# Kernel tuning notes

Hardware: AMD Instinct MI355X
Metric: run time of the kernel (lower is better)

Reference implementation:

```python
import jax, jax.numpy as jnp
import numpy as np

N = 100000
E = 3200000
IN_F = 256
OUT_F = 64
ALPHA = 0.2  # LeakyReLU negative slope


def setup_inputs() -> dict:
    key = jax.random.key(0)
    k1, k2, k3, k4 = jax.random.split(key, 4)
    adj = jax.random.randint(k1, (2, E), 0, N, dtype=jnp.int64)
    x = jax.random.normal(k2, (N, IN_F), dtype=jnp.float32)
    # xavier-normal-ish scales
    W_fc = jax.random.normal(k3, (OUT_F, IN_F), dtype=jnp.float32) * (1.414 * np.sqrt(2.0 / (IN_F + OUT_F)))
    b_fc = jnp.zeros((OUT_F,), dtype=jnp.float32)
    a = jax.random.normal(k4, (1, 2 * OUT_F), dtype=jnp.float32) * (1.414 * np.sqrt(2.0 / (1 + 2 * OUT_F)))
    return {"adj": adj, "x": x, "W_fc": W_fc, "b_fc": b_fc, "a": a}


def reference(adj, x, W_fc, b_fc, a):
    src = adj[0]  # [E]
    dst = adj[1]  # [E]
    h = x @ W_fc.T + b_fc                       # [N, OUT_F]
    a1, a2 = a[0, :OUT_F], a[0, OUT_F:]         # split of attention vector
    # e = leakyrelu(a . [h_src || h_dst]) computed without materializing concat
    s1 = h @ a1                                  # [N]
    s2 = h @ a2                                  # [N]
    e = s1[src] + s2[dst]                        # [E]
    e = jnp.where(e > 0, e, ALPHA * e)           # LeakyReLU
    # dgl edge_softmax: softmax over edges grouped by destination node
    m = jax.ops.segment_max(e, dst, num_segments=N)     # [N]
    ex = jnp.exp(e - m[dst])                             # [E]
    denom = jax.ops.segment_sum(ex, dst, num_segments=N) # [N]
    att = ex / denom[dst]                                # [E]
    # SparseTensor(row=src, col=dst, value=att) @ h -> out[src] += att * h[dst]
    h_prime = jax.ops.segment_sum(att[:, None] * h[dst], src, num_segments=N)  # [N, OUT_F]
    return jax.nn.elu(h_prime)  # concat=True branch
```

## Files before the change

kernel.cpp:

```cpp
#include <hip/hip_runtime.h>
#include <math.h>

#define N_NODES 100000
#define N_EDGES 3200000
#define IN_F 256
#define OUT_F 64
#define LRELU_ALPHA 0.2f
#define NBKT 782
#define CAP 4480

typedef unsigned short u16;
typedef __attribute__((ext_vector_type(8))) short short8;
typedef __attribute__((ext_vector_type(4))) float floatx4;

__device__ inline u16 f2bf(float f) {
  unsigned u = __float_as_uint(f);
  u += 0x7FFFu + ((u >> 16) & 1u);
  return (u16)(u >> 16);
}
__device__ inline float bf2f(u16 h) {
  return __uint_as_float(((unsigned)h) << 16);
}

__global__ __launch_bounds__(256) void k_prep(const float* __restrict__ W,
                                              u16* __restrict__ Wbf,
                                              int* __restrict__ sfill,
                                              int* __restrict__ dfill) {
  if (blockIdx.x < 64) {
    int i = blockIdx.x * 256 + threadIdx.x;
    Wbf[i] = f2bf(W[i]);
  } else {
    for (int i = threadIdx.x; i < NBKT; i += 256) {
      sfill[i] = 0;
      dfill[i] = 0;
    }
  }
}

__global__ __launch_bounds__(256) void k_linear(
    const float* __restrict__ x, const u16* __restrict__ Wbf,
    const float* __restrict__ b, const float* __restrict__ a,
    u16* __restrict__ hbf, float* __restrict__ s1, float* __restrict__ s2) {
  __shared__ u16 Wlds[64 * 264];

  const int t = threadIdx.x;
#pragma unroll
  for (int p = 0; p < 8; p++) {
    int c = p * 256 + t;
    int row = c >> 5;
    int kc = (c & 31) * 8;
    *(short8*)&Wlds[row * 264 + kc] = *(const short8*)&Wbf[row * 256 + kc];
  }
  __syncthreads();

  const int w = t >> 6;
  const int lane = t & 63;
  const int col = lane & 15;
  const int q = lane >> 4;
  const int m0 = blockIdx.x * 64 + w * 16;

  floatx4 acc[4];
#pragma unroll
  for (int nt = 0; nt < 4; nt++) acc[nt] = (floatx4){0.f, 0.f, 0.f, 0.f};

  int mrow = m0 + col;
  if (mrow > N_NODES - 1) mrow = N_NODES - 1;
  const float* xrow = x + (size_t)mrow * IN_F + q * 8;

#pragma unroll
  for (int kk = 0; kk < 8; kk++) {
    float4 f0 = *(const float4*)(xrow + kk * 32);
    float4 f1 = *(const float4*)(xrow + kk * 32 + 4);
    short8 af;
    af[0] = (short)f2bf(f0.x);
    af[1] = (short)f2bf(f0.y);
    af[2] = (short)f2bf(f0.z);
    af[3] = (short)f2bf(f0.w);
    af[4] = (short)f2bf(f1.x);
    af[5] = (short)f2bf(f1.y);
    af[6] = (short)f2bf(f1.z);
    af[7] = (short)f2bf(f1.w);
#pragma unroll
    for (int nt = 0; nt < 4; nt++) {
      short8 bfr = *(const short8*)&Wlds[(nt * 16 + col) * 264 + kk * 32 + q * 8];
      acc[nt] = __builtin_amdgcn_mfma_f32_16x16x32_bf16(af, bfr, acc[nt], 0, 0, 0);
    }
  }

  float bv[4], a1v[4], a2v[4];
#pragma unroll
  for (int nt = 0; nt < 4; nt++) {
    bv[nt] = b[nt * 16 + col];
    a1v[nt] = a[nt * 16 + col];
    a2v[nt] = a[OUT_F + nt * 16 + col];
  }
#pragma unroll
  for (int r = 0; r < 4; r++) {
    int node = m0 + q * 4 + r;
    float p1 = 0.f, p2 = 0.f;
#pragma unroll
    for (int nt = 0; nt < 4; nt++) {
      float hv = acc[nt][r] + bv[nt];
      if (node < N_NODES) hbf[(size_t)node * OUT_F + nt * 16 + col] = f2bf(hv);
      p1 = fmaf(hv, a1v[nt], p1);
      p2 = fmaf(hv, a2v[nt], p2);
    }
#pragma unroll
    for (int s = 1; s < 16; s <<= 1) {
      p1 += __shfl_xor(p1, s, 16);
      p2 += __shfl_xor(p2, s, 16);
    }
    if (col == 0 && node < N_NODES) {
      s1[node] = p1;
      s2[node] = p2;
    }
  }
}

#define PBT 512
#define EPT_P 8
#define PEB (PBT * EPT_P)
__global__ __launch_bounds__(PBT) void k_place(
    const int* __restrict__ src, const int* __restrict__ dst,
    const float* __restrict__ s1, const float* __restrict__ s2,
    int* __restrict__ sfill, int* __restrict__ dfill,
    float2* __restrict__ pairS, float2* __restrict__ pairD) {
  __shared__ int lc[NBKT];
  __shared__ int ofs[NBKT];
  __shared__ int gbase[NBKT];
  __shared__ int tot;
  __shared__ float2 stage[PEB];
  __shared__ u16 stageB[PEB];

  const int t = threadIdx.x;
  const int base = blockIdx.x * PEB + t;

  float ex[EPT_P];
  int pk[EPT_P];
  int bs[EPT_P];

  for (int i = t; i < NBKT; i += PBT) lc[i] = 0;
  if (t == 0) tot = 0;
  __syncthreads();

#pragma unroll
  for (int j = 0; j < EPT_P; j++) {
    int e = base + j * PBT;
    if (e < N_EDGES) {
      int s = src[e];
      int d = dst[e];
      float v = s1[s] + s2[d];
      v = v > 0.f ? v : LRELU_ALPHA * v;
      ex[j] = __expf(v);
      pk[j] = d | ((s & 127) << 17);
      bs[j] = s >> 7;
      atomicAdd(&lc[bs[j]], 1);
    } else {
      bs[j] = -1;
    }
  }
  __syncthreads();

  for (int i = t; i < NBKT; i += PBT) {
    int c = lc[i];
    if (c) {
      gbase[i] = i * CAP + atomicAdd(&sfill[i], c);
      ofs[i] = atomicAdd(&tot, c);
    }
  }
  __syncthreads();
  const int nval = tot;
  for (int i = t; i < NBKT; i += PBT) lc[i] = 0;
  __syncthreads();

#pragma unroll
  for (int j = 0; j < EPT_P; j++) {
    if (bs[j] >= 0) {
      int r = atomicAdd(&lc[bs[j]], 1);
      int idx = ofs[bs[j]] + r;
      stage[idx] = make_float2(ex[j], __int_as_float(pk[j]));
      stageB[idx] = (u16)bs[j];
    }
  }
  __syncthreads();

  for (int i = t; i < nval; i += PBT) {
    int bkt = stageB[i];
    pairS[gbase[bkt] + (i - ofs[bkt])] = stage[i];
  }
  __syncthreads();

  for (int i = t; i < NBKT; i += PBT) lc[i] = 0;
  if (t == 0) tot = 0;
  __syncthreads();
#pragma unroll
  for (int j = 0; j < EPT_P; j++) {
    if (bs[j] >= 0) {
      int bd = (pk[j] & 0x1FFFF) >> 7;
      atomicAdd(&lc[bd], 1);
    }
  }
  __syncthreads();

  for (int i = t; i < NBKT; i += PBT) {
    int c = lc[i];
    if (c) {
      gbase[i] = i * CAP + atomicAdd(&dfill[i], c);
      ofs[i] = atomicAdd(&tot, c);
    }
  }
  __syncthreads();
  for (int i = t; i < NBKT; i += PBT) lc[i] = 0;
  __syncthreads();

#pragma unroll
  for (int j = 0; j < EPT_P; j++) {
    if (bs[j] >= 0) {
      int d = pk[j] & 0x1FFFF;
      int bd = d >> 7;
      int r = atomicAdd(&lc[bd], 1);
      int idx = ofs[bd] + r;
      stage[idx] = make_float2(ex[j], __int_as_float(d & 127));
      stageB[idx] = (u16)bd;
    }
  }
  __syncthreads();

  for (int i = t; i < nval; i += PBT) {
    int bkt = stageB[i];
    pairD[gbase[bkt] + (i - ofs[bkt])] = stage[i];
  }
}

__global__ __launch_bounds__(256) void k_denom(const int* __restrict__ dfill,
                                               const float2* __restrict__ pairD,
                                               float* __restrict__ denom_r) {
  __shared__ float lacc[128];
  const int t = threadIdx.x;
  const int bkt = blockIdx.x;
  if (t < 128) lacc[t] = 0.f;
  __syncthreads();
  int beg = bkt * CAP;
  int end = beg + dfill[bkt];
  for (int i = beg + t; i < end; i += 256) {
    float2 p = pairD[i];
    atomicAdd(&lacc[__float_as_int(p.y)], p.x);
  }
  __syncthreads();
  if (t < 128) {
    int node = bkt * 128 + t;
    if (node < N_NODES) denom_r[node] = 1.0f / lacc[t];
  }
}

#define SAT 512
__global__ __launch_bounds__(SAT) void k_sortagg(
    const int* __restrict__ sfill, const float2* __restrict__ pairS,
    const float* __restrict__ denom_r, const u16* __restrict__ hbf,
    float* __restrict__ out) {
  __shared__ float2 stg[CAP];
  __shared__ int lcnt[128];
  __shared__ int cur[128];
  __shared__ int nbeg[128];
  __shared__ int nend[128];
  __shared__ int w0tot;
  const int t = threadIdx.x;
  const int bkt = blockIdx.x;

  if (t < 128) lcnt[t] = 0;
  __syncthreads();

  const int gbeg = bkt * CAP;
  const int ne = sfill[bkt];

  for (int i = t; i < ne; i += SAT) {
    int pkv = __float_as_int(pairS[gbeg + i].y);
    atomicAdd(&lcnt[(pkv >> 17) & 127], 1);
  }
  __syncthreads();

  const int lane = t & 63;
  int v = (t < 128) ? lcnt[t] : 0;
  int val = v;
#pragma unroll
  for (int o = 1; o < 64; o <<= 1) {
    int u = __shfl_up(val, o, 64);
    if (lane >= o) val += u;
  }
  if (t == 63) w0tot = val;
  __syncthreads();
  if (t < 128) {
    int excl = val - v + ((t >= 64) ? w0tot : 0);
    cur[t] = excl;
    nbeg[t] = excl;
    nend[t] = excl + v;
  }
  __syncthreads();

  for (int i = t; i < ne; i += SAT) {
    float2 p = pairS[gbeg + i];
    int pkv = __float_as_int(p.y);
    int sl = (pkv >> 17) & 127;
    int d = pkv & 0x1FFFF;
    float att = p.x * denom_r[d];
    int pos = atomicAdd(&cur[sl], 1);
    stg[pos] = make_float2(att, __int_as_float(d));
  }
  __syncthreads();

  const int G = t >> 4;
  const int sl = t & 15;
  for (int nl = G; nl < 128; nl += 32) {
    int node = bkt * 128 + nl;
    int i = nbeg[nl];
    const int e0 = nend[nl];
    float4 acc = make_float4(0.f, 0.f, 0.f, 0.f);
    for (; i + 1 < e0; i += 2) {
      float2 p0 = stg[i];
      float2 p1 = stg[i + 1];
      int d0 = __float_as_int(p0.y);
      int d1 = __float_as_int(p1.y);
      ushort4 q0 = *(const ushort4*)&hbf[(size_t)d0 * OUT_F + sl * 4];
      ushort4 q1 = *(const ushort4*)&hbf[(size_t)d1 * OUT_F + sl * 4];
      acc.x = fmaf(p0.x, bf2f(q0.x), acc.x);
      acc.y = fmaf(p0.x, bf2f(q0.y), acc.y);
      acc.z = fmaf(p0.x, bf2f(q0.z), acc.z);
      acc.w = fmaf(p0.x, bf2f(q0.w), acc.w);
      acc.x = fmaf(p1.x, bf2f(q1.x), acc.x);
      acc.y = fmaf(p1.x, bf2f(q1.y), acc.y);
      acc.z = fmaf(p1.x, bf2f(q1.z), acc.z);
      acc.w = fmaf(p1.x, bf2f(q1.w), acc.w);
    }
    if (i < e0) {
      float2 p = stg[i];
      int d = __float_as_int(p.y);
      ushort4 q = *(const ushort4*)&hbf[(size_t)d * OUT_F + sl * 4];
      acc.x = fmaf(p.x, bf2f(q.x), acc.x);
      acc.y = fmaf(p.x, bf2f(q.y), acc.y);
      acc.z = fmaf(p.x, bf2f(q.z), acc.z);
      acc.w = fmaf(p.x, bf2f(q.w), acc.w);
    }
    if (node < N_NODES) {
      float4 o;
      o.x = acc.x > 0.f ? acc.x : expm1f(acc.x);
      o.y = acc.y > 0.f ? acc.y : expm1f(acc.y);
      o.z = acc.z > 0.f ? acc.z : expm1f(acc.z);
      o.w = acc.w > 0.f ? acc.w : expm1f(acc.w);
      *(float4*)(out + (size_t)node * OUT_F + sl * 4) = o;
    }
  }
}

extern "C" void kernel_launch(void* const* d_in, const int* in_sizes, int n_in,
                              void* d_out, int out_size, void* d_ws,
                              size_t ws_size, hipStream_t stream) {
  const int* adj = (const int*)d_in[0];
  const float* x = (const float*)d_in[1];
  const float* W = (const float*)d_in[2];
  const float* b = (const float*)d_in[3];
  const float* a = (const float*)d_in[4];
  float* out = (float*)d_out;

  float* ws = (float*)d_ws;
  float* s1v = ws;
  float* s2v = ws + 100000;
  float* denom_r = ws + 200000;
  int* sfill = (int*)(ws + 300000);
  int* dfill = (int*)(ws + 300800);
  float2* pairS = (float2*)(ws + 301600);
  float2* pairD = (float2*)(ws + 7308320);
  u16* hbf = (u16*)(ws + 14315040);
  u16* Wbf = (u16*)(ws + 17515040);

  const int* src = adj;
  const int* dst = adj + N_EDGES;

  k_prep<<<65, 256, 0, stream>>>(W, Wbf, sfill, dfill);
  k_linear<<<(N_NODES + 63) / 64, 256, 0, stream>>>(x, Wbf, b, a, hbf, s1v, s2v);
  k_place<<<(N_EDGES + PEB - 1) / PEB, PBT, 0, stream>>>(
      src, dst, s1v, s2v, sfill, dfill, pairS, pairD);
  k_denom<<<NBKT, 256, 0, stream>>>(dfill, pairD, denom_r);
  k_sortagg<<<NBKT, SAT, 0, stream>>>(sfill, pairS, denom_r, hbf, out);
}
```

Measured before the change: 369.9 us.

## Split edge placement into two grid halves and pack dst-side pairs into 32 bits

The placement kernel now runs on a 2-D grid: one half of the blocks buckets edges by source, the other by destination, instead of each block doing both passes in sequence. This doubles block-level parallelism and drops the second set of barriers, but every edge's src/dst indices and s1/s2 scores are now read twice and the exponential is computed twice. The destination-side records are packed into 32 bits, with the exp value in bf16 and the local node index in the low bits. This halves pairD traffic for the placement and denominator kernels, at the cost of bf16 precision in the softmax denominator.

```diff
diff --git a/kernel.cpp b/kernel.cpp
--- a/kernel.cpp
+++ b/kernel.cpp
@@ -124,7 +124,7 @@
     const int* __restrict__ src, const int* __restrict__ dst,
     const float* __restrict__ s1, const float* __restrict__ s2,
     int* __restrict__ sfill, int* __restrict__ dfill,
-    float2* __restrict__ pairS, float2* __restrict__ pairD) {
+    float2* __restrict__ pairS, unsigned* __restrict__ pairD) {
   __shared__ int lc[NBKT];
   __shared__ int ofs[NBKT];
   __shared__ int gbase[NBKT];
@@ -133,11 +133,12 @@
   __shared__ u16 stageB[PEB];
 
   const int t = threadIdx.x;
+  const int side = blockIdx.y;
   const int base = blockIdx.x * PEB + t;
 
   float ex[EPT_P];
-  int pk[EPT_P];
-  int bs[EPT_P];
+  int key[EPT_P];
+  int bk[EPT_P];
 
   for (int i = t; i < NBKT; i += PBT) lc[i] = 0;
   if (t == 0) tot = 0;
@@ -152,19 +153,25 @@
       float v = s1[s] + s2[d];
       v = v > 0.f ? v : LRELU_ALPHA * v;
       ex[j] = __expf(v);
-      pk[j] = d | ((s & 127) << 17);
-      bs[j] = s >> 7;
-      atomicAdd(&lc[bs[j]], 1);
+      if (side == 0) {
+        key[j] = d | ((s & 127) << 17);
+        bk[j] = s >> 7;
+      } else {
+        key[j] = d & 127;
+        bk[j] = d >> 7;
+      }
+      atomicAdd(&lc[bk[j]], 1);
     } else {
-      bs[j] = -1;
-    }
-  }
-  __syncthreads();
-
+      bk[j] = -1;
+    }
+  }
+  __syncthreads();
+
+  int* fill = side ? dfill : sfill;
   for (int i = t; i < NBKT; i += PBT) {
     int c = lc[i];
     if (c) {
-      gbase[i] = i * CAP + atomicAdd(&sfill[i], c);
+      gbase[i] = i * CAP + atomicAdd(&fill[i], c);
       ofs[i] = atomicAdd(&tot, c);
     }
   }
@@ -173,67 +180,42 @@
   for (int i = t; i < NBKT; i += PBT) lc[i] = 0;
   __syncthreads();
 
-#pragma unroll
-  for (int j = 0; j < EPT_P; j++) {
-    if (bs[j] >= 0) {
-      int r = atomicAdd(&lc[bs[j]], 1);
-      int idx = ofs[bs[j]] + r;
-      stage[idx] = make_float2(ex[j], __int_as_float(pk[j]));
-      stageB[idx] = (u16)bs[j];
-    }
-  }
-  __syncthreads();
-
-  for (int i = t; i < nval; i += PBT) {
-    int bkt = stageB[i];
-    pairS[gbase[bkt] + (i - ofs[bkt])] = stage[i];
-  }
-  __syncthreads();
-
-  for (int i = t; i < NBKT; i += PBT) lc[i] = 0;
-  if (t == 0) tot = 0;
-  __syncthreads();
-#pragma unroll
-  for (int j = 0; j < EPT_P; j++) {
-    if (bs[j] >= 0) {
-      int bd = (pk[j] & 0x1FFFF) >> 7;
-      atomicAdd(&lc[bd], 1);
-    }
-  }
-  __syncthreads();
-
-  for (int i = t; i < NBKT; i += PBT) {
-    int c = lc[i];
-    if (c) {
-      gbase[i] = i * CAP + atomicAdd(&dfill[i], c);
-      ofs[i] = atomicAdd(&tot, c);
-    }
-  }
-  __syncthreads();
-  for (int i = t; i < NBKT; i += PBT) lc[i] = 0;
-  __syncthreads();
-
-#pragma unroll
-  for (int j = 0; j < EPT_P; j++) {
-    if (bs[j] >= 0) {
-      int d = pk[j] & 0x1FFFF;
-      int bd = d >> 7;
-      int r = atomicAdd(&lc[bd], 1);
-      int idx = ofs[bd] + r;
-      stage[idx] = make_float2(ex[j], __int_as_float(d & 127));
-      stageB[idx] = (u16)bd;
-    }
-  }
-  __syncthreads();
-
-  for (int i = t; i < nval; i += PBT) {
-    int bkt = stageB[i];
-    pairD[gbase[bkt] + (i - ofs[bkt])] = stage[i];
+  if (side == 0) {
+#pragma unroll
+    for (int j = 0; j < EPT_P; j++) {
+      if (bk[j] >= 0) {
+        int r = atomicAdd(&lc[bk[j]], 1);
+        int idx = ofs[bk[j]] + r;
+        stage[idx] = make_float2(ex[j], __int_as_float(key[j]));
+        stageB[idx] = (u16)bk[j];
+      }
+    }
+    __syncthreads();
+    for (int i = t; i < nval; i += PBT) {
+      int bkt = stageB[i];
+      pairS[gbase[bkt] + (i - ofs[bkt])] = stage[i];
+    }
+  } else {
+    unsigned* stg32 = (unsigned*)stage;
+#pragma unroll
+    for (int j = 0; j < EPT_P; j++) {
+      if (bk[j] >= 0) {
+        int r = atomicAdd(&lc[bk[j]], 1);
+        int idx = ofs[bk[j]] + r;
+        stg32[idx] = ((unsigned)f2bf(ex[j]) << 16) | (unsigned)key[j];
+        stageB[idx] = (u16)bk[j];
+      }
+    }
+    __syncthreads();
+    for (int i = t; i < nval; i += PBT) {
+      int bkt = stageB[i];
+      pairD[gbase[bkt] + (i - ofs[bkt])] = stg32[i];
+    }
   }
 }
 
 __global__ __launch_bounds__(256) void k_denom(const int* __restrict__ dfill,
-                                               const float2* __restrict__ pairD,
+                                               const unsigned* __restrict__ pairD,
                                                float* __restrict__ denom_r) {
   __shared__ float lacc[128];
   const int t = threadIdx.x;
@@ -243,8 +225,8 @@
   int beg = bkt * CAP;
   int end = beg + dfill[bkt];
   for (int i = beg + t; i < end; i += 256) {
-    float2 p = pairD[i];
-    atomicAdd(&lacc[__float_as_int(p.y)], p.x);
+    unsigned u = pairD[i];
+    atomicAdd(&lacc[u & 127], __uint_as_float(u & 0xFFFF0000u));
   }
   __syncthreads();
   if (t < 128) {
@@ -368,16 +350,16 @@
   int* sfill = (int*)(ws + 300000);
   int* dfill = (int*)(ws + 300800);
   float2* pairS = (float2*)(ws + 301600);
-  float2* pairD = (float2*)(ws + 7308320);
-  u16* hbf = (u16*)(ws + 14315040);
-  u16* Wbf = (u16*)(ws + 17515040);
+  unsigned* pairD = (unsigned*)(ws + 7308320);
+  u16* hbf = (u16*)(ws + 10811680);
+  u16* Wbf = (u16*)(ws + 14011680);
 
   const int* src = adj;
   const int* dst = adj + N_EDGES;
 
   k_prep<<<65, 256, 0, stream>>>(W, Wbf, sfill, dfill);
   k_linear<<<(N_NODES + 63) / 64, 256, 0, stream>>>(x, Wbf, b, a, hbf, s1v, s2v);
-  k_place<<<(N_EDGES + PEB - 1) / PEB, PBT, 0, stream>>>(
+  k_place<<<dim3((N_EDGES + PEB - 1) / PEB, 2), PBT, 0, stream>>>(
       src, dst, s1v, s2v, sfill, dfill, pairS, pairD);
   k_denom<<<NBKT, 256, 0, stream>>>(dfill, pairD, denom_r);
   k_sortagg<<<NBKT, SAT, 0, stream>>>(sfill, pairS, denom_r, hbf, out);
```

Measured after the change: 365.5 us. About the same (-1.2%).
